# Kernel optimization log

Hardware: AMD Instinct MI355X
Metric: run time of the kernel (lower is better)

The kernel has to match this reference:

```python
import jax, jax.numpy as jnp
import numpy as np

NUM_LAYERS = 3
NORM = True


def wl_refine(colors, src, dst, n):
    """One WLConv step: new color = first-occurrence rank of the signature
    (own_color, sorted multiset of in-neighbor colors). Exact partition match
    with PyG WLConv (fresh hashmap per layer, as each conv is called once)."""
    nbr = colors[src]                                  # [E] neighbor colors grouped by dst
    deg = jnp.zeros((n,), jnp.int32).at[dst].add(1)    # in-degree
    maxdeg = int(deg.max())
    order = jnp.lexsort((nbr, dst))                    # sort edges by (dst, nbr_color)
    d_s, c_s = dst[order], nbr[order]
    offsets = jnp.cumsum(deg) - deg                    # start of each node's edge block
    pos = jnp.arange(d_s.shape[0]) - offsets[d_s]      # rank within block (already color-sorted)
    mat = jnp.full((n, maxdeg), -1, colors.dtype).at[d_s, pos].set(c_s)
    keys = jnp.concatenate([colors[:, None], mat], axis=1)  # [n, maxdeg+1] signatures
    uniq, first, inv = jnp.unique(keys, axis=0, return_index=True, return_inverse=True)
    inv = inv.reshape(-1)
    rank = jnp.argsort(jnp.argsort(first))             # unique-id -> first-occurrence order id
    return rank[inv], int(uniq.shape[0])


def histogram(colors, num_colors, batch, bsize, weights, norm):
    """PyG WLConv.histogram: scatter counts into [bsize, num_colors], L2-normalize rows."""
    idx = batch * num_colors + colors
    out = jnp.zeros((bsize * num_colors,), weights.dtype).at[idx].add(weights)
    out = out.reshape(bsize, num_colors)
    if norm:
        out = out / jnp.linalg.norm(out, axis=-1, keepdims=True)
    return out


def setup_inputs() -> dict:
    key = jax.random.key(0)
    k1, k2, k3 = jax.random.split(key, 3)
    N, E, B, C0 = 100000, 3200000, 512, 32
    x = jax.random.randint(k1, (N,), 0, C0)
    edge_index = jax.random.randint(k2, (2, E), 0, N)
    batch = jnp.sort(jax.random.randint(k3, (N,), 0, B))
    node_weight = jnp.ones((N,), jnp.float32)
    return {"x": x, "edge_index": edge_index, "batch": batch, "node_weight": node_weight}


def reference(x, edge_index, batch, node_weight):
    src, dst = edge_index[0], edge_index[1]            # PyG WLConv: neighbors of i = sources of edges into i
    n = x.shape[0]
    bsize = int(batch.max()) + 1
    colors = x
    hists = []
    for _ in range(NUM_LAYERS):
        colors, nc = wl_refine(colors, src, dst, n)
        hists.append(histogram(colors, nc, batch, bsize, node_weight, NORM))
    return tuple(hists)
```

## Files before the change

### kernel.cpp

```cpp
#include <hip/hip_runtime.h>
#include <math.h>

#define WL_LAYERS 3
#define HSLOTS (1u << 18)
#define HMASK  (HSLOTS - 1u)
#define SCHUNK 1024
#define MAXD 128

typedef unsigned long long u64;

__device__ __forceinline__ u64 mix64(u64 x) {
    x += 0x9e3779b97f4a7c15ULL;
    x = (x ^ (x >> 30)) * 0xbf58476d1ce4e5b9ULL;
    x = (x ^ (x >> 27)) * 0x94d049bb133111ebULL;
    return x ^ (x >> 31);
}

__global__ void k_setup(int* __restrict__ cursor, u64* __restrict__ ktabs,
                        int* __restrict__ gmins, float* __restrict__ sumsqs,
                        int* __restrict__ dcnt, long long* __restrict__ scalars, int n) {
    int i = blockIdx.x * blockDim.x + threadIdx.x;
    int T = gridDim.x * blockDim.x;
    for (int j = i; j < n; j += T) cursor[j] = 0;
    int HT = 3 * (int)HSLOTS;
    for (int j = i; j < HT; j += T) { ktabs[j] = 0ULL; gmins[j] = 0x7fffffff; }
    for (int j = i; j < 3 * n; j += T) sumsqs[j] = 0.f;
    if (i < 8) dcnt[i] = 0;
    if (i == 0) scalars[3] = 0;
}

__global__ void k_scatter(const int* __restrict__ src, const int* __restrict__ dst,
                          int* __restrict__ cursor, int* __restrict__ adj,
                          float* __restrict__ zbuf, long long zn, int E) {
    int e = blockIdx.x * blockDim.x + threadIdx.x;
    int T = gridDim.x * blockDim.x;
    if (e < E) {
        int d = dst[e];
        int pos = atomicAdd(&cursor[d], 1);
        if (pos < MAXD) adj[d * MAXD + pos] = src[e];
    }
    long long n4 = zn >> 2;
    float4* z4 = (float4*)zbuf;
    for (long long j = e; j < n4; j += (long long)T)
        z4[j] = make_float4(0.f, 0.f, 0.f, 0.f);
    if (e < (int)(zn & 3)) zbuf[(n4 << 2) + e] = 0.f;
}

__device__ __forceinline__ void hash_insert_body(
        const int* __restrict__ col, const int* __restrict__ cursor,
        const int* __restrict__ adj, u64* __restrict__ ktab, int* __restrict__ gmin,
        int* __restrict__ nodeslot, int n) {
    int i = blockIdx.x * 256 + threadIdx.x;
    if (i >= n) return;
    int dg = cursor[i];
    if (dg > MAXD) dg = MAXD;
    int s0 = i * MAXD;
    u64 h = 0ULL;
    for (int k = 0; k < dg; ++k) {
        u64 c = (u64)(unsigned)col[adj[s0 + k]];
        h += mix64(c ^ 0x5bf03635c1d4aeb1ULL);
    }
    u64 bb = mix64((u64)(unsigned)col[i] + 0x0123456789abcdefULL);
    u64 cc = mix64((u64)(unsigned)dg + 0xfedcba9876543210ULL);
    u64 sig = mix64(h + bb * 0x9e3779b97f4a7c15ULL + cc * 0xc2b2ae3d27d4eb4fULL);
    if (!sig) sig = 1;
    unsigned slot = (unsigned)sig & HMASK;
    for (;;) {
        u64 p = atomicCAS(&ktab[slot], 0ULL, sig);
        if (p == 0ULL || p == sig) break;
        slot = (slot + 1) & HMASK;
    }
    nodeslot[i] = slot;
    atomicMin(&gmin[slot], i);
}

__global__ void k_hashinsert(const int* __restrict__ col, const int* __restrict__ cursor,
                             const int* __restrict__ adj, u64* __restrict__ ktab,
                             int* __restrict__ gmin, int* __restrict__ nodeslot, int n) {
    hash_insert_body(col, cursor, adj, ktab, gmin, nodeslot, n);
}

__global__ void k_scanF(const int* __restrict__ nodeslot, const int* __restrict__ gmin,
                        int* __restrict__ rankv, int* __restrict__ bsum,
                        int* __restrict__ dcnt, long long* __restrict__ scalars,
                        int layer, const int* __restrict__ batch, int n, int nb) {
    __shared__ int s[256];
    __shared__ int sh_last;
    int t = threadIdx.x;
    int idx0 = blockIdx.x * SCHUNK + t * 4;
    int v[4]; int sum = 0;
#pragma unroll
    for (int j = 0; j < 4; ++j) {
        int ii = idx0 + j;
        v[j] = (ii < n && gmin[nodeslot[ii]] == ii) ? 1 : 0;
        sum += v[j];
    }
    s[t] = sum; __syncthreads();
    for (int off = 1; off < 256; off <<= 1) {
        int x = (t >= off) ? s[t - off] : 0;
        __syncthreads(); s[t] += x; __syncthreads();
    }
    int run = s[t] - sum;
#pragma unroll
    for (int j = 0; j < 4; ++j) { int ii = idx0 + j; if (ii < n) rankv[ii] = run; run += v[j]; }
    if (t == 255) bsum[blockIdx.x] = s[255];
    __threadfence();
    if (t == 0) sh_last = (atomicAdd(&dcnt[0], 1) == gridDim.x - 1);
    __syncthreads();
    if (sh_last) {
        __threadfence();
        int v2 = (t < nb) ? bsum[t] : 0;
        __syncthreads();
        s[t] = v2; __syncthreads();
        for (int off = 1; off < 256; off <<= 1) {
            int x = (t >= off) ? s[t - off] : 0;
            __syncthreads(); s[t] += x; __syncthreads();
        }
        if (t < nb) bsum[t] = s[t] - v2;
        if (t == 255) {
            long long total = s[255];
            scalars[layer] = total;
            long long bsize = (long long)batch[n - 1] + 1;
            scalars[4 + layer] = scalars[3 + layer] + bsize * total;
        }
    }
}

__global__ void k_hist(const int* __restrict__ batch, const int* __restrict__ nodeslot,
                       const int* __restrict__ gmin, const int* __restrict__ rankv,
                       const int* __restrict__ bsum, int* __restrict__ nxt,
                       const float* __restrict__ w, float* __restrict__ out,
                       float* __restrict__ sumsq, float* __restrict__ oldv,
                       const long long* __restrict__ scalars, int layer, int n) {
    __shared__ float ssq[64];
    __shared__ int rbase_s;
    int t = threadIdx.x;
    int i = blockIdx.x * 256 + t;
    if (t < 64) ssq[t] = 0.f;
    if (t == 0) {
        int a = blockIdx.x * 256;
        rbase_s = batch[a < n ? a : n - 1];
    }
    __syncthreads();
    if (i < n) {
        int g = gmin[nodeslot[i]];
        int c = rankv[g] + bsum[g >> 10];
        nxt[i] = c;
        int r = batch[i];
        long long idx = scalars[3 + layer] + (long long)r * scalars[layer] + c;
        float wi = w[i];
        float old = atomicAdd(&out[idx], wi);
        oldv[i] = old;
        float val = 2.f * old * wi + wi * wi;
        int sl = r - rbase_s;
        if (sl >= 0 && sl < 64) atomicAdd(&ssq[sl], val);
        else atomicAdd(&sumsq[r], val);
    }
    __syncthreads();
    if (t < 64 && ssq[t] != 0.f) atomicAdd(&sumsq[rbase_s + t], ssq[t]);
}

__global__ void k_normhash(
        const int* __restrict__ batch, const int* __restrict__ col,
        float* __restrict__ out, const float* __restrict__ sumsq_prev,
        const float* __restrict__ oldv, const long long* __restrict__ scalars,
        int layerPrev, const int* __restrict__ cursor, const int* __restrict__ adj,
        u64* __restrict__ ktab, int* __restrict__ gmin, int* __restrict__ nodeslot,
        int n) {
    int i = blockIdx.x * 256 + threadIdx.x;
    if (i < n && oldv[i] == 0.f) {
        int r = batch[i];
        long long idx = scalars[3 + layerPrev] + (long long)r * scalars[layerPrev] + col[i];
        out[idx] = out[idx] / sqrtf(sumsq_prev[r]);
    }
    hash_insert_body(col, cursor, adj, ktab, gmin, nodeslot, n);
}

__global__ void k_norm(const int* __restrict__ batch, const int* __restrict__ col,
                       float* __restrict__ out, const float* __restrict__ sumsq,
                       const float* __restrict__ oldv,
                       const long long* __restrict__ scalars, int layer, int n) {
    int i = blockIdx.x * blockDim.x + threadIdx.x;
    if (i >= n) return;
    if (oldv[i] != 0.f) return;
    int r = batch[i];
    long long idx = scalars[3 + layer] + (long long)r * scalars[layer] + col[i];
    out[idx] = out[idx] / sqrtf(sumsq[r]);
}

extern "C" void kernel_launch(void* const* d_in, const int* in_sizes, int n_in,
                              void* d_out, int out_size, void* d_ws, size_t ws_size,
                              hipStream_t stream) {
    const int* x = (const int*)d_in[0];
    const int* ei = (const int*)d_in[1];
    const int* batch = (const int*)d_in[2];
    const float* w = (const float*)d_in[3];
    int N = in_sizes[0];
    int E = in_sizes[1] / 2;
    const int* src = ei;
    const int* dst = ei + E;

    char* p = (char*)d_ws;
    u64* ktabs = (u64*)p;               p += (size_t)3 * HSLOTS * 8;
    long long* scalars = (long long*)p; p += 8 * 8;
    int* adj      = (int*)p;            p += (size_t)N * MAXD * 4;
    int* gmins    = (int*)p;            p += (size_t)3 * HSLOTS * 4;
    int* cursor   = (int*)p;            p += (size_t)N * 4;
    int* nodeslot = (int*)p;            p += (size_t)N * 4;
    int* rankv    = (int*)p;            p += (size_t)N * 4;
    int* colA     = (int*)p;            p += (size_t)N * 4;
    int* colB     = (int*)p;            p += (size_t)N * 4;
    float* oldv   = (float*)p;          p += (size_t)N * 4;
    float* sumsqs = (float*)p;          p += (size_t)3 * N * 4;
    int* bsum     = (int*)p;            p += 256 * 4;
    int* dcnt     = (int*)p;            p += 8 * 4;
    if ((size_t)(p - (char*)d_ws) > ws_size) return;

    int gN = (N + 255) / 256;
    int gE = (E + 255) / 256;
    int nb = (N + SCHUNK - 1) / SCHUNK;
    if (nb > 256) return;

    float* out = (float*)d_out;
    long long zn = (long long)out_size;

    k_setup<<<gE, 256, 0, stream>>>(cursor, ktabs, gmins, sumsqs, dcnt, scalars, N);
    k_scatter<<<gE, 256, 0, stream>>>(src, dst, cursor, adj, out, zn, E);
    k_hashinsert<<<gN, 256, 0, stream>>>(x, cursor, adj, ktabs, gmins, nodeslot, N);

    int* nxt = colA;
    for (int l = 0; l < WL_LAYERS; ++l) {
        u64* kt = ktabs + (size_t)l * HSLOTS;
        int* gm = gmins + (size_t)l * HSLOTS;
        float* sq = sumsqs + (size_t)l * N;
        k_scanF<<<nb, 256, 0, stream>>>(nodeslot, gm, rankv, bsum, dcnt + l,
                                        scalars, l, batch, N, nb);
        k_hist<<<gN, 256, 0, stream>>>(batch, nodeslot, gm, rankv, bsum, nxt, w,
                                       out, sq, oldv, scalars, l, N);
        if (l < WL_LAYERS - 1) {
            k_normhash<<<gN, 256, 0, stream>>>(batch, nxt, out, sq, oldv,
                                               scalars, l, cursor, adj,
                                               kt + HSLOTS, gm + HSLOTS, nodeslot, N);
        } else {
            k_norm<<<gN, 256, 0, stream>>>(batch, nxt, out, sq, oldv, scalars, l, N);
        }
        nxt = (l == 0) ? colB : colA;
    }
}
```

Measured before the change: 462.1 us.

## Spread output zeroing and per-layer table init across kernels, vectorize edge loads

Result: faster. 383.7 us (median of 2 runs) (-17.0%).

```diff
diff --git a/kernel.cpp b/kernel.cpp
--- a/kernel.cpp
+++ b/kernel.cpp
@@ -8,6 +8,7 @@
 #define MAXD 128
 
 typedef unsigned long long u64;
+typedef int v4i __attribute__((ext_vector_type(4)));
 
 __device__ __forceinline__ u64 mix64(u64 x) {
     x += 0x9e3779b97f4a7c15ULL;
@@ -16,34 +17,55 @@
     return x ^ (x >> 31);
 }
 
-__global__ void k_setup(int* __restrict__ cursor, u64* __restrict__ ktabs,
-                        int* __restrict__ gmins, float* __restrict__ sumsqs,
-                        int* __restrict__ dcnt, long long* __restrict__ scalars, int n) {
-    int i = blockIdx.x * blockDim.x + threadIdx.x;
-    int T = gridDim.x * blockDim.x;
-    for (int j = i; j < n; j += T) cursor[j] = 0;
-    int HT = 3 * (int)HSLOTS;
-    for (int j = i; j < HT; j += T) { ktabs[j] = 0ULL; gmins[j] = 0x7fffffff; }
-    for (int j = i; j < 3 * n; j += T) sumsqs[j] = 0.f;
-    if (i < 8) dcnt[i] = 0;
-    if (i == 0) scalars[3] = 0;
+__device__ __forceinline__ void nt_fill(float* __restrict__ zbuf, long long a4,
+                                        long long b4, long long tid, long long T) {
+    v4i z = {0, 0, 0, 0};
+    v4i* z4 = (v4i*)zbuf;
+    for (long long j = a4 + tid; j < b4; j += T)
+        __builtin_nontemporal_store(z, &z4[j]);
+}
+
+__global__ void k_setup(int* __restrict__ cursor, u64* __restrict__ ktab0,
+                        int* __restrict__ gmin0, float* __restrict__ sumsq0,
+                        int* __restrict__ dcnt, long long* __restrict__ scalars,
+                        float* __restrict__ zbuf, long long a4e, long long zn, int n) {
+    long long tid = (long long)blockIdx.x * blockDim.x + threadIdx.x;
+    long long T = (long long)gridDim.x * blockDim.x;
+    for (long long j = tid; j < n; j += T) cursor[j] = 0;
+    for (long long j = tid; j < (long long)HSLOTS; j += T) { ktab0[j] = 0ULL; gmin0[j] = 0x7fffffff; }
+    for (long long j = tid; j < n; j += T) sumsq0[j] = 0.f;
+    if (tid < 8) dcnt[tid] = 0;
+    if (tid == 0) scalars[3] = 0;
+    nt_fill(zbuf, 0, a4e, tid, T);
+    long long n4 = zn >> 2;
+    if (tid < (zn & 3)) zbuf[(n4 << 2) + tid] = 0.f;
 }
 
 __global__ void k_scatter(const int* __restrict__ src, const int* __restrict__ dst,
                           int* __restrict__ cursor, int* __restrict__ adj,
-                          float* __restrict__ zbuf, long long zn, int E) {
-    int e = blockIdx.x * blockDim.x + threadIdx.x;
-    int T = gridDim.x * blockDim.x;
-    if (e < E) {
-        int d = dst[e];
-        int pos = atomicAdd(&cursor[d], 1);
-        if (pos < MAXD) adj[d * MAXD + pos] = src[e];
-    }
-    long long n4 = zn >> 2;
-    float4* z4 = (float4*)zbuf;
-    for (long long j = e; j < n4; j += (long long)T)
-        z4[j] = make_float4(0.f, 0.f, 0.f, 0.f);
-    if (e < (int)(zn & 3)) zbuf[(n4 << 2) + e] = 0.f;
+                          float* __restrict__ zbuf, long long a4, long long b4, int E) {
+    long long tid = (long long)blockIdx.x * blockDim.x + threadIdx.x;
+    long long T = (long long)gridDim.x * blockDim.x;
+    if ((E & 3) == 0) {
+        int nE4 = E >> 2;
+        if (tid < nE4) {
+            v4i s4 = ((const v4i*)src)[tid];
+            v4i d4 = ((const v4i*)dst)[tid];
+#pragma unroll
+            for (int j = 0; j < 4; ++j) {
+                int d = d4[j];
+                int pos = atomicAdd(&cursor[d], 1);
+                if (pos < MAXD) adj[(size_t)d * MAXD + pos] = s4[j];
+            }
+        }
+    } else {
+        for (long long e = tid; e < E; e += T) {
+            int d = dst[e];
+            int pos = atomicAdd(&cursor[d], 1);
+            if (pos < MAXD) adj[(size_t)d * MAXD + pos] = src[e];
+        }
+    }
+    nt_fill(zbuf, a4, b4, tid, T);
 }
 
 __device__ __forceinline__ void hash_insert_body(
@@ -52,12 +74,21 @@
         int* __restrict__ nodeslot, int n) {
     int i = blockIdx.x * 256 + threadIdx.x;
     if (i >= n) return;
-    int dg = cursor[i];
-    if (dg > MAXD) dg = MAXD;
-    int s0 = i * MAXD;
+    int dg = cursor[i]; if (dg > MAXD) dg = MAXD;
+    const int* row = adj + (size_t)i * MAXD;
     u64 h = 0ULL;
-    for (int k = 0; k < dg; ++k) {
-        u64 c = (u64)(unsigned)col[adj[s0 + k]];
+    int dg4 = dg >> 2;
+    const v4i* row4 = (const v4i*)row;
+    for (int k4 = 0; k4 < dg4; ++k4) {
+        v4i r = row4[k4];
+#pragma unroll
+        for (int j = 0; j < 4; ++j) {
+            u64 c = (u64)(unsigned)col[r[j]];
+            h += mix64(c ^ 0x5bf03635c1d4aeb1ULL);
+        }
+    }
+    for (int k = dg4 << 2; k < dg; ++k) {
+        u64 c = (u64)(unsigned)col[row[k]];
         h += mix64(c ^ 0x5bf03635c1d4aeb1ULL);
     }
     u64 bb = mix64((u64)(unsigned)col[i] + 0x0123456789abcdefULL);
@@ -76,7 +107,10 @@
 
 __global__ void k_hashinsert(const int* __restrict__ col, const int* __restrict__ cursor,
                              const int* __restrict__ adj, u64* __restrict__ ktab,
-                             int* __restrict__ gmin, int* __restrict__ nodeslot, int n) {
+                             int* __restrict__ gmin, int* __restrict__ nodeslot,
+                             float* __restrict__ zbuf, long long b4, long long n4, int n) {
+    long long tid = (long long)blockIdx.x * 256 + threadIdx.x;
+    nt_fill(zbuf, b4, n4, tid, (long long)gridDim.x * 256);
     hash_insert_body(col, cursor, adj, ktab, gmin, nodeslot, n);
 }
 
@@ -131,11 +165,18 @@
                        const int* __restrict__ bsum, int* __restrict__ nxt,
                        const float* __restrict__ w, float* __restrict__ out,
                        float* __restrict__ sumsq, float* __restrict__ oldv,
-                       const long long* __restrict__ scalars, int layer, int n) {
+                       const long long* __restrict__ scalars, int layer,
+                       u64* __restrict__ ktabN, int* __restrict__ gminN,
+                       float* __restrict__ sumsqN, int zeroNext, int n) {
     __shared__ float ssq[64];
     __shared__ int rbase_s;
     int t = threadIdx.x;
     int i = blockIdx.x * 256 + t;
+    if (zeroNext) {
+        int tid = i, T = gridDim.x * 256;
+        for (int j = tid; j < (int)HSLOTS; j += T) { ktabN[j] = 0ULL; gminN[j] = 0x7fffffff; }
+        for (int j = tid; j < n; j += T) sumsqN[j] = 0.f;
+    }
     if (t < 64) ssq[t] = 0.f;
     if (t == 0) {
         int a = blockIdx.x * 256;
@@ -218,25 +259,33 @@
 
     int gN = (N + 255) / 256;
     int gE = (E + 255) / 256;
+    int gE4 = ((E + 3) / 4 + 255) / 256;
     int nb = (N + SCHUNK - 1) / SCHUNK;
     if (nb > 256) return;
 
     float* out = (float*)d_out;
     long long zn = (long long)out_size;
-
-    k_setup<<<gE, 256, 0, stream>>>(cursor, ktabs, gmins, sumsqs, dcnt, scalars, N);
-    k_scatter<<<gE, 256, 0, stream>>>(src, dst, cursor, adj, out, zn, E);
-    k_hashinsert<<<gN, 256, 0, stream>>>(x, cursor, adj, ktabs, gmins, nodeslot, N);
+    long long n4 = zn >> 2;
+    long long A = (n4 * 3) / 10;
+    long long B = (n4 * 9) / 10;
+
+    k_setup<<<gE, 256, 0, stream>>>(cursor, ktabs, gmins, sumsqs, dcnt, scalars,
+                                    out, A, zn, N);
+    k_scatter<<<gE4, 256, 0, stream>>>(src, dst, cursor, adj, out, A, B, E);
+    k_hashinsert<<<gN, 256, 0, stream>>>(x, cursor, adj, ktabs, gmins, nodeslot,
+                                         out, B, n4, N);
 
     int* nxt = colA;
     for (int l = 0; l < WL_LAYERS; ++l) {
         u64* kt = ktabs + (size_t)l * HSLOTS;
         int* gm = gmins + (size_t)l * HSLOTS;
         float* sq = sumsqs + (size_t)l * N;
+        int zeroNext = (l < WL_LAYERS - 1) ? 1 : 0;
         k_scanF<<<nb, 256, 0, stream>>>(nodeslot, gm, rankv, bsum, dcnt + l,
                                         scalars, l, batch, N, nb);
         k_hist<<<gN, 256, 0, stream>>>(batch, nodeslot, gm, rankv, bsum, nxt, w,
-                                       out, sq, oldv, scalars, l, N);
+                                       out, sq, oldv, scalars, l,
+                                       kt + HSLOTS, gm + HSLOTS, sq + N, zeroNext, N);
         if (l < WL_LAYERS - 1) {
             k_normhash<<<gN, 256, 0, stream>>>(batch, nxt, out, sq, oldv,
                                                scalars, l, cursor, adj,
```
